# Kernel optimization log

Measured on AMD Instinct MI355X. Metric: run time of the kernel, lower is better.

Reference implementation:

```python
import jax, jax.numpy as jnp
import numpy as np

D_MODEL = 2048
D_STATE = 128
D_CONV = 4
EXPAND = 2
HEADDIM = 64
CHUNK = 64
D_INNER = EXPAND * D_MODEL            # 4096
NHEADS = D_INNER // HEADDIM           # 64
CONV_DIM = D_INNER + 2 * D_STATE      # 4352
D_IN_PROJ = 2 * D_INNER + 2 * D_STATE + NHEADS  # 8512
BATCH, SEQLEN = 2, 2048


def segsum(x):
    """Stable segment sum. x: (..., T) -> (..., T, T)."""
    T = x.shape[-1]
    xx = jnp.broadcast_to(x[..., :, None], x.shape + (T,))  # [.., d, e] = x[.., d]
    mask_lower = jnp.tril(jnp.ones((T, T), dtype=bool), -1)
    s = jnp.cumsum(jnp.where(mask_lower, xx, 0.0), axis=-2)
    mask_diag = jnp.tril(jnp.ones((T, T), dtype=bool), 0)
    return jnp.where(mask_diag, s, -jnp.inf)


def ssd(x, A, Bm, Cm, chunk):
    """x: [b,L,h,p], A: [b,L,h], Bm/Cm: [b,L,n]."""
    b, L, h, p = x.shape
    c = L // chunk
    x = x.reshape(b, c, chunk, h, p)
    A = A.reshape(b, c, chunk, h).transpose(0, 3, 1, 2)     # b h c l
    Bm = Bm.reshape(b, c, chunk, -1)                         # b c l n
    Cm = Cm.reshape(b, c, chunk, -1)
    A_cum = jnp.cumsum(A, axis=-1)                           # b h c l
    Lmat = jnp.exp(segsum(A))                                # b h c l s
    # intra-chunk (diagonal) output
    Y_diag = jnp.einsum('bcln,bcsn,bhcls,bcshp->bclhp', Cm, Bm, Lmat, x)
    # per-chunk states
    decay_states = jnp.exp(A_cum[..., -1:] - A_cum)          # b h c l
    states = jnp.einsum('bcln,bhcl,bclhp->bchpn', Bm, decay_states, x)
    init = jnp.zeros_like(states[:, :1])
    states = jnp.concatenate([init, states], axis=1)         # b (c+1) h p n
    # inter-chunk recurrence via segsum over chunk-level decays
    A_last = jnp.pad(A_cum[..., -1], ((0, 0), (0, 0), (1, 0)))  # b h (c+1)
    decay_chunk = jnp.exp(segsum(A_last))                    # b h (c+1) (c+1)
    new_states = jnp.einsum('bhzc,bchpn->bzhpn', decay_chunk, states)
    states, final_state = new_states[:, :-1], new_states[:, -1]
    # state -> output
    out_decay = jnp.exp(A_cum)                               # b h c l
    Y_off = jnp.einsum('bcln,bchpn,bhcl->bclhp', Cm, states, out_decay)
    return (Y_diag + Y_off).reshape(b, L, h, p), final_state


def setup_inputs() -> dict:
    key = jax.random.key(0)
    ks = jax.random.split(key, 8)
    u = jax.random.normal(ks[0], (BATCH, SEQLEN, D_MODEL), jnp.float32)
    W_in = jax.random.normal(ks[1], (D_MODEL, D_IN_PROJ), jnp.float32) / np.sqrt(D_MODEL).astype(np.float32)
    conv_w = jax.random.normal(ks[2], (CONV_DIM, D_CONV), jnp.float32) * np.sqrt(2.0 / D_CONV).astype(np.float32)
    conv_b = jnp.zeros((CONV_DIM,), jnp.float32)
    dt_bias = jax.random.uniform(ks[3], (NHEADS,), jnp.float32, minval=-2.0, maxval=2.0)
    A_log = jax.random.normal(ks[4], (NHEADS,), jnp.float32) * 0.1
    D_param = jnp.ones((NHEADS,), jnp.float32)
    norm_w = jnp.ones((D_INNER,), jnp.float32)
    W_out = jax.random.normal(ks[5], (D_INNER, D_MODEL), jnp.float32) / np.sqrt(D_INNER).astype(np.float32)
    return {'u': u, 'W_in': W_in, 'conv_w': conv_w, 'conv_b': conv_b,
            'dt_bias': dt_bias, 'A_log': A_log, 'D_param': D_param,
            'norm_w': norm_w, 'W_out': W_out}


def reference(u, W_in, conv_w, conv_b, dt_bias, A_log, D_param, norm_w, W_out):
    b, L, _ = u.shape
    zxbcdt = u @ W_in                                        # [b, L, 2*din + 2*n + h]
    z = zxbcdt[..., :D_INNER]
    xBC = zxbcdt[..., D_INNER:D_INNER + CONV_DIM]
    dt = zxbcdt[..., D_INNER + CONV_DIM:]
    dt = jax.nn.softplus(dt + dt_bias)                       # [b, L, h]
    # causal depthwise conv1d (kernel D_CONV, groups=channels)
    xp = jnp.pad(xBC, ((0, 0), (D_CONV - 1, 0), (0, 0)))
    xBC = sum(xp[:, w:w + L, :] * conv_w[:, w] for w in range(D_CONV)) + conv_b
    xBC = jax.nn.silu(xBC)
    x = xBC[..., :D_INNER]
    Bm = xBC[..., D_INNER:D_INNER + D_STATE]                 # [b, L, n]
    Cm = xBC[..., D_INNER + D_STATE:]                        # [b, L, n]
    x = x.reshape(b, L, NHEADS, HEADDIM)
    A = -jnp.exp(A_log)                                      # [h]
    y, final_state = ssd(x * dt[..., None], A * dt, Bm, Cm, CHUNK)
    y = y + x * D_param[:, None]                             # skip term
    y = y.reshape(b, L, D_INNER)
    # gated RMSNorm (fp32)
    yf = y * jax.nn.silu(z)
    rrms = jax.lax.rsqrt(jnp.mean(yf * yf, axis=-1, keepdims=True) + 1e-5)
    y = yf * rrms * norm_w
    return y @ W_out
```

## Files before the change

kernel.cpp:

```cpp
#include <hip/hip_runtime.h>

typedef unsigned short u16;
typedef __attribute__((ext_vector_type(8))) short bhalf8;
typedef __attribute__((ext_vector_type(4))) float floatx4;

__device__ __forceinline__ u16 f2bf(float f) {
    union { float f; unsigned u; } v; v.f = f;
    unsigned u = v.u;
    unsigned r = u + 0x7fffu + ((u >> 16) & 1u);
    return (u16)(r >> 16);
}
__device__ __forceinline__ float b2f(u16 h) {
    union { unsigned u; float f; } v; v.u = ((unsigned)h) << 16; return v.f;
}
__device__ __forceinline__ void unpack2(unsigned u, float& lo, float& hi) {
    union { unsigned u; float f; } a, b;
    a.u = u << 16; b.u = u & 0xffff0000u;
    lo = a.f; hi = b.f;
}
__device__ __forceinline__ void load_lds16(const void* g, void* l) {
    __builtin_amdgcn_global_load_lds(
        (const __attribute__((address_space(1))) unsigned int*)g,
        (__attribute__((address_space(3))) unsigned int*)l, 16, 0, 0);
}

__global__ void k_f2b4(const float* __restrict__ in, u16* __restrict__ out, int n4) {
    int i = blockIdx.x * 256 + threadIdx.x;
    if (i < n4) {
        float4 v = ((const float4*)in)[i];
        unsigned lo = (unsigned)f2bf(v.x) | ((unsigned)f2bf(v.y) << 16);
        unsigned hi = (unsigned)f2bf(v.z) | ((unsigned)f2bf(v.w) << 16);
        ((uint2*)out)[i] = make_uint2(lo, hi);
    }
}

__global__ void k_transpose_f2b(const float* __restrict__ W, u16* __restrict__ Wt,
                                int K, int N) {
    __shared__ float tile[32][33];
    int nt = blockIdx.x * 32, kt = blockIdx.y * 32;
    int tx = threadIdx.x, ty = threadIdx.y;
    #pragma unroll
    for (int r = 0; r < 32; r += 8) {
        int k = kt + ty + r, n = nt + tx;
        tile[ty + r][tx] = (n < N && k < K) ? W[(size_t)k * N + n] : 0.f;
    }
    __syncthreads();
    #pragma unroll
    for (int r = 0; r < 32; r += 8) {
        int n = nt + ty + r, k = kt + tx;
        Wt[(size_t)n * K + k] = f2bf(tile[tx][ty + r]);
    }
}

template <int EPI>
__global__ __launch_bounds__(256) void gemm_bt(
    const u16* __restrict__ A, const u16* __restrict__ Bt, int M, int N, int K,
    float* __restrict__ outF,
    u16* __restrict__ zb, u16* __restrict__ xbc, float* __restrict__ dtq,
    const float* __restrict__ dt_bias) {
    __shared__ u16 As[128 * 64];
    __shared__ u16 Bs[128 * 64];
    int t = threadIdx.x;
    int w = t >> 6, lane = t & 63;
    int m0 = blockIdx.y * 128, n0 = blockIdx.x * 128;
    int wm = (w >> 1) * 64, wn = (w & 1) * 64;
    floatx4 acc[4][4];
    #pragma unroll
    for (int i = 0; i < 4; i++)
        #pragma unroll
        for (int j = 0; j < 4; j++) acc[i][j] = (floatx4){0.f, 0.f, 0.f, 0.f};

    for (int k0 = 0; k0 < K; k0 += 64) {
        #pragma unroll
        for (int i = 0; i < 4; i++) {
            int c = w * 4 + i;
            int byte = c * 1024 + lane * 16;
            int row = byte >> 7;
            int colb = (byte & 127) ^ ((row & 7) << 4);
            load_lds16(A + (size_t)(m0 + row) * K + k0 + (colb >> 1), (char*)As + byte);
            load_lds16(Bt + (size_t)(n0 + row) * K + k0 + (colb >> 1), (char*)Bs + byte);
        }
        __syncthreads();
        #pragma unroll
        for (int ks = 0; ks < 2; ks++) {
            int kk = ks * 32 + ((lane >> 4) << 3);
            bhalf8 af[4], bf[4];
            #pragma unroll
            for (int mi = 0; mi < 4; mi++) {
                int row = wm + mi * 16 + (lane & 15);
                int idx = (row * 64 + kk) ^ ((row & 7) << 3);
                af[mi] = *(const bhalf8*)(As + idx);
            }
            #pragma unroll
            for (int ni = 0; ni < 4; ni++) {
                int col = wn + ni * 16 + (lane & 15);
                int idx = (col * 64 + kk) ^ ((col & 7) << 3);
                bf[ni] = *(const bhalf8*)(Bs + idx);
            }
            #pragma unroll
            for (int mi = 0; mi < 4; mi++)
                #pragma unroll
                for (int ni = 0; ni < 4; ni++)
                    acc[mi][ni] = __builtin_amdgcn_mfma_f32_16x16x32_bf16(
                        af[mi], bf[ni], acc[mi][ni], 0, 0, 0);
        }
        __syncthreads();
    }
    #pragma unroll
    for (int mi = 0; mi < 4; mi++) {
        #pragma unroll
        for (int ni = 0; ni < 4; ni++) {
            floatx4 v = acc[mi][ni];
            int col = n0 + wn + ni * 16 + (lane & 15);
            #pragma unroll
            for (int r = 0; r < 4; r++) {
                int row = m0 + wm + mi * 16 + ((lane >> 4) << 2) + r;
                float val = v[r];
                if (EPI == 0) {
                    outF[(size_t)row * N + col] = val;
                } else {
                    if (col < 4096) {
                        zb[(size_t)row * 4096 + col] = f2bf(val);
                    } else if (col < 8448) {
                        xbc[(size_t)row * 4352 + (col - 4096)] = f2bf(val);
                    } else if (col < 8512) {
                        int h = col - 8448;
                        float xv = val + dt_bias[h];
                        float sp = (xv > 20.f) ? xv : log1pf(__expf(xv));
                        dtq[(size_t)row * 64 + h] = sp;
                    }
                }
            }
        }
    }
}

__global__ __launch_bounds__(256) void k_conv(
    const u16* __restrict__ xbc, const float* __restrict__ conv_w,
    const float* __restrict__ conv_b,
    u16* __restrict__ x, u16* __restrict__ Bo, u16* __restrict__ Co) {
    int row = blockIdx.x;
    int b = row >> 11, l = row & 2047;
    for (int ch = threadIdx.x; ch < 4352; ch += 256) {
        float acc = conv_b[ch];
        #pragma unroll
        for (int w = 0; w < 4; w++) {
            int ll = l - 3 + w;
            if (ll >= 0) acc += b2f(xbc[(size_t)(b * 2048 + ll) * 4352 + ch]) * conv_w[ch * 4 + w];
        }
        float v = acc / (1.f + __expf(-acc));
        if (ch < 4096) {
            x[(size_t)row * 4096 + ch] = f2bf(v);
        } else if (ch < 4224) {
            Bo[(size_t)row * 128 + (ch - 4096)] = f2bf(v);
        } else {
            Co[(size_t)row * 128 + (ch - 4224)] = f2bf(v);
        }
    }
}

__global__ void k_dtprep(const float* __restrict__ dtq, const float* __restrict__ A_log,
                         float* __restrict__ acum, float* __restrict__ Tc) {
    int bc = blockIdx.x;
    int h = threadIdx.x;
    float A = -__expf(A_log[h]);
    float s = 0.f;
    #pragma unroll
    for (int l = 0; l < 64; l++) {
        int row = bc * 64 + l;
        s += A * dtq[row * 64 + h];
        acum[(size_t)row * 64 + h] = s;
    }
    int b = bc >> 5, c = bc & 31;
    Tc[(b * 64 + h) * 32 + c] = s;
}

__global__ __launch_bounds__(256) void k_G(const u16* __restrict__ Bo, const u16* __restrict__ Co,
                                           float* __restrict__ G) {
    int bc = blockIdx.x;
    __shared__ float BsT[128][68];
    __shared__ float Cs[64][132];
    int t = threadIdx.x;
    for (int idx = t; idx < 64 * 128; idx += 256) {
        int r = idx >> 7, n = idx & 127;
        BsT[n][r] = b2f(Bo[(size_t)(bc * 64 + r) * 128 + n]);
        Cs[r][n] = b2f(Co[(size_t)(bc * 64 + r) * 128 + n]);
    }
    __syncthreads();
    int l = t >> 2, sq = t & 3;
    float a[16];
    #pragma unroll
    for (int i = 0; i < 16; i++) a[i] = 0.f;
    for (int n = 0; n < 128; n++) {
        float cv = Cs[l][n];
        const float4* bp = (const float4*)&BsT[n][sq * 16];
        float4 b0 = bp[0], b1 = bp[1], b2 = bp[2], b3 = bp[3];
        a[0] += cv * b0.x; a[1] += cv * b0.y; a[2] += cv * b0.z; a[3] += cv * b0.w;
        a[4] += cv * b1.x; a[5] += cv * b1.y; a[6] += cv * b1.z; a[7] += cv * b1.w;
        a[8] += cv * b2.x; a[9] += cv * b2.y; a[10] += cv * b2.z; a[11] += cv * b2.w;
        a[12] += cv * b3.x; a[13] += cv * b3.y; a[14] += cv * b3.z; a[15] += cv * b3.w;
    }
    size_t gb = ((size_t)bc * 64 + l) * 64 + sq * 16;
    #pragma unroll
    for (int i = 0; i < 16; i++) G[gb + i] = a[i];
}

__global__ __launch_bounds__(256) void k_diag(
    const u16* __restrict__ xb, const u16* __restrict__ Bo,
    const float* __restrict__ G, const float* __restrict__ acum,
    const float* __restrict__ dtq,
    u16* __restrict__ y, u16* __restrict__ cs) {
    int bc = blockIdx.x, h = blockIdx.y;
    __shared__ u16 XT[4096];
    __shared__ u16 Pl[4096];
    __shared__ u16 BTd[8192];
    __shared__ float ac[64], dec[64], dts[64];
    int t = threadIdx.x, w = t >> 6, lane = t & 63;
    if (t < 64) {
        ac[t] = acum[(size_t)(bc * 64 + t) * 64 + h];
        dts[t] = dtq[(size_t)(bc * 64 + t) * 64 + h];
    }
    __syncthreads();
    if (t < 64) dec[t] = __expf(ac[63] - ac[t]);
    for (int idx = t; idx < 4096; idx += 256) {
        int s = idx >> 6, p = idx & 63;
        float v = b2f(xb[(size_t)(bc * 64 + s) * 4096 + h * 64 + p]) * dts[s];
        XT[(p << 6) + (s ^ ((p & 7) << 3))] = f2bf(v);
    }
    for (int idx = t; idx < 4096; idx += 256) {
        int l = idx >> 6, s = idx & 63;
        float v = (s <= l) ? __expf(ac[l] - ac[s]) * G[((size_t)bc * 64 + l) * 64 + s] : 0.f;
        Pl[(l << 6) + (s ^ ((l & 7) << 3))] = f2bf(v);
    }
    __syncthreads();
    for (int idx = t; idx < 8192; idx += 256) {
        int l = idx >> 7, n = idx & 127;
        float v = b2f(Bo[(size_t)(bc * 64 + l) * 128 + n]) * dec[l];
        BTd[(n << 6) + (l ^ ((n & 7) << 3))] = f2bf(v);
    }
    __syncthreads();
    {
        floatx4 accY[4];
        #pragma unroll
        for (int ni = 0; ni < 4; ni++) accY[ni] = (floatx4){0.f, 0.f, 0.f, 0.f};
        int row = (w << 4) + (lane & 15);
        #pragma unroll
        for (int ks = 0; ks < 2; ks++) {
            int k = (ks << 5) + ((lane >> 4) << 3);
            int kx = k ^ ((row & 7) << 3);
            bhalf8 af = *(const bhalf8*)(Pl + (row << 6) + kx);
            #pragma unroll
            for (int ni = 0; ni < 4; ni++) {
                int pr = (ni << 4) + (lane & 15);
                bhalf8 bf = *(const bhalf8*)(XT + (pr << 6) + kx);
                accY[ni] = __builtin_amdgcn_mfma_f32_16x16x32_bf16(af, bf, accY[ni], 0, 0, 0);
            }
        }
        #pragma unroll
        for (int ni = 0; ni < 4; ni++) {
            int col = (ni << 4) + (lane & 15);
            #pragma unroll
            for (int r = 0; r < 4; r++) {
                int l = (w << 4) + ((lane >> 4) << 2) + r;
                y[(size_t)(bc * 64 + l) * 4096 + h * 64 + col] = f2bf(accY[ni][r]);
            }
        }
    }
    {
        floatx4 accS[8];
        #pragma unroll
        for (int ni = 0; ni < 8; ni++) accS[ni] = (floatx4){0.f, 0.f, 0.f, 0.f};
        int prow = (w << 4) + (lane & 15);
        #pragma unroll
        for (int ks = 0; ks < 2; ks++) {
            int k = (ks << 5) + ((lane >> 4) << 3);
            int kx = k ^ ((prow & 7) << 3);
            bhalf8 af = *(const bhalf8*)(XT + (prow << 6) + kx);
            #pragma unroll
            for (int ni = 0; ni < 8; ni++) {
                int nr = (ni << 4) + (lane & 15);
                bhalf8 bf = *(const bhalf8*)(BTd + (nr << 6) + kx);
                accS[ni] = __builtin_amdgcn_mfma_f32_16x16x32_bf16(af, bf, accS[ni], 0, 0, 0);
            }
        }
        #pragma unroll
        for (int ni = 0; ni < 8; ni++) {
            int n = (ni << 4) + (lane & 15);
            #pragma unroll
            for (int r = 0; r < 4; r++) {
                int p = (w << 4) + ((lane >> 4) << 2) + r;
                cs[((size_t)(bc * 64 + h) * 64 + p) * 128 + n] = f2bf(accS[ni][r]);
            }
        }
    }
}

__global__ __launch_bounds__(256) void k_scan(u16* __restrict__ cs, const float* __restrict__ Tc) {
    int bid = blockIdx.x;
    int bh = bid >> 5, pb = bid & 31;
    int b = bh >> 6, h = bh & 63;
    int pn = pb * 256 + threadIdx.x;
    const float* Tp = Tc + bh * 32;
    size_t stride = (size_t)64 * 8192;
    size_t base = (((size_t)(b * 32) * 64) + h) * 8192 + pn;
    float v[32];
    #pragma unroll
    for (int c = 0; c < 32; c++) v[c] = b2f(cs[base + (size_t)c * stride]);
    float P = 0.f;
    #pragma unroll
    for (int c = 0; c < 32; c++) {
        float tmp = v[c];
        cs[base + (size_t)c * stride] = f2bf(P);
        P = __expf(Tp[c]) * P + tmp;
    }
}

__global__ __launch_bounds__(256) void k_yoff(
    const u16* __restrict__ Co, const u16* __restrict__ cs,
    const float* __restrict__ acum, u16* __restrict__ y) {
    int bc = blockIdx.x, h = blockIdx.y;
    __shared__ u16 Cl[8192];
    __shared__ u16 Sl[8192];
    __shared__ float od[64];
    int t = threadIdx.x, w = t >> 6, lane = t & 63;
    for (int idx = t; idx < 8192; idx += 256) {
        int l = idx >> 7, n = idx & 127;
        Cl[(l << 7) + (n ^ ((l & 15) << 3))] = Co[(size_t)(bc * 64 + l) * 128 + n];
    }
    size_t pbase = ((size_t)bc * 64 + h) * 8192;
    for (int idx = t; idx < 8192; idx += 256) {
        int p = idx >> 7, n = idx & 127;
        Sl[(p << 7) + (n ^ ((p & 15) << 3))] = cs[pbase + idx];
    }
    if (t < 64) od[t] = __expf(acum[(size_t)(bc * 64 + t) * 64 + h]);
    __syncthreads();
    floatx4 acc[4];
    #pragma unroll
    for (int ni = 0; ni < 4; ni++) acc[ni] = (floatx4){0.f, 0.f, 0.f, 0.f};
    int lrow = (w << 4) + (lane & 15);
    #pragma unroll
    for (int ks = 0; ks < 4; ks++) {
        int k = (ks << 5) + ((lane >> 4) << 3);
        int kx = k ^ ((lrow & 15) << 3);
        bhalf8 af = *(const bhalf8*)(Cl + (lrow << 7) + kx);
        #pragma unroll
        for (int ni = 0; ni < 4; ni++) {
            int pr = (ni << 4) + (lane & 15);
            bhalf8 bf = *(const bhalf8*)(Sl + (pr << 7) + kx);
            acc[ni] = __builtin_amdgcn_mfma_f32_16x16x32_bf16(af, bf, acc[ni], 0, 0, 0);
        }
    }
    #pragma unroll
    for (int ni = 0; ni < 4; ni++) {
        int col = (ni << 4) + (lane & 15);
        #pragma unroll
        for (int r = 0; r < 4; r++) {
            int l = (w << 4) + ((lane >> 4) << 2) + r;
            size_t yi = (size_t)(bc * 64 + l) * 4096 + h * 64 + col;
            y[yi] = f2bf(b2f(y[yi]) + od[l] * acc[ni][r]);
        }
    }
}

__global__ __launch_bounds__(256) void k_norm(
    const u16* __restrict__ y, const u16* __restrict__ x, const u16* __restrict__ z,
    const float* __restrict__ D_param, const float* __restrict__ norm_w,
    u16* __restrict__ ynorm) {
    int row = blockIdx.x;
    int t = threadIdx.x;
    size_t base = (size_t)row * 4096 + (size_t)t * 16;
    float yv[16], xf[16], zf[16];
    {
        uint4 a = ((const uint4*)(y + base))[0];
        uint4 b = ((const uint4*)(y + base))[1];
        unpack2(a.x, yv[0], yv[1]); unpack2(a.y, yv[2], yv[3]);
        unpack2(a.z, yv[4], yv[5]); unpack2(a.w, yv[6], yv[7]);
        unpack2(b.x, yv[8], yv[9]); unpack2(b.y, yv[10], yv[11]);
        unpack2(b.z, yv[12], yv[13]); unpack2(b.w, yv[14], yv[15]);
    }
    {
        uint4 a = ((const uint4*)(x + base))[0];
        uint4 b = ((const uint4*)(x + base))[1];
        unpack2(a.x, xf[0], xf[1]); unpack2(a.y, xf[2], xf[3]);
        unpack2(a.z, xf[4], xf[5]); unpack2(a.w, xf[6], xf[7]);
        unpack2(b.x, xf[8], xf[9]); unpack2(b.y, xf[10], xf[11]);
        unpack2(b.z, xf[12], xf[13]); unpack2(b.w, xf[14], xf[15]);
    }
    {
        uint4 a = ((const uint4*)(z + base))[0];
        uint4 b = ((const uint4*)(z + base))[1];
        unpack2(a.x, zf[0], zf[1]); unpack2(a.y, zf[2], zf[3]);
        unpack2(a.z, zf[4], zf[5]); unpack2(a.w, zf[6], zf[7]);
        unpack2(b.x, zf[8], zf[9]); unpack2(b.y, zf[10], zf[11]);
        unpack2(b.z, zf[12], zf[13]); unpack2(b.w, zf[14], zf[15]);
    }
    float D = D_param[t >> 2];
    float vals[16], ss = 0.f;
    #pragma unroll
    for (int j = 0; j < 16; j++) {
        float v = yv[j] + xf[j] * D;
        float zz = zf[j];
        float yf = v * (zz / (1.f + __expf(-zz)));
        vals[j] = yf;
        ss += yf * yf;
    }
    #pragma unroll
    for (int o = 32; o > 0; o >>= 1) ss += __shfl_down(ss, o, 64);
    __shared__ float red[4];
    if ((t & 63) == 0) red[t >> 6] = ss;
    __syncthreads();
    float tot = red[0] + red[1] + red[2] + red[3];
    float rr = rsqrtf(tot * (1.f / 4096.f) + 1e-5f);
    unsigned o32[8];
    #pragma unroll
    for (int j = 0; j < 8; j++) {
        float lo = vals[2 * j] * rr * norm_w[t * 16 + 2 * j];
        float hi = vals[2 * j + 1] * rr * norm_w[t * 16 + 2 * j + 1];
        o32[j] = (unsigned)f2bf(lo) | ((unsigned)f2bf(hi) << 16);
    }
    uint4 w0, w1;
    w0.x = o32[0]; w0.y = o32[1]; w0.z = o32[2]; w0.w = o32[3];
    w1.x = o32[4]; w1.y = o32[5]; w1.z = o32[6]; w1.w = o32[7];
    ((uint4*)(ynorm + base))[0] = w0;
    ((uint4*)(ynorm + base))[1] = w1;
}

extern "C" void kernel_launch(void* const* d_in, const int* in_sizes, int n_in,
                              void* d_out, int out_size, void* d_ws, size_t ws_size,
                              hipStream_t stream) {
    const float* u       = (const float*)d_in[0];
    const float* W_in    = (const float*)d_in[1];
    const float* conv_w  = (const float*)d_in[2];
    const float* conv_b  = (const float*)d_in[3];
    const float* dt_bias = (const float*)d_in[4];
    const float* A_log   = (const float*)d_in[5];
    const float* D_param = (const float*)d_in[6];
    const float* norm_w  = (const float*)d_in[7];
    const float* W_out   = (const float*)d_in[8];
    float* out = (float*)d_out;

    const size_t REGION = (size_t)134217728;
    size_t need = REGION
                + (size_t)33554432
                + (size_t)33554432
                + (size_t)1048576
                + (size_t)1048576
                + (size_t)1048576
                + (size_t)16384
                + (size_t)1048576
                + (size_t)1048576
                + (size_t)33554432;
    if (ws_size < need) return;

    char* ws = (char*)d_ws;
    u16*   ubf   = (u16*)(ws);
    u16*   WinT  = (u16*)(ws + 16777216);
    u16*   xbc   = (u16*)(ws + 16777216 + 35651584);
    u16*   cs    = (u16*)(ws);
    u16*   WoutT = (u16*)(ws);
    u16*   ynorm = (u16*)(ws + 16777216);
    char* p = ws + REGION;
    u16*   zb    = (u16*)p;            p += 33554432;
    u16*   xb    = (u16*)p;            p += 33554432;
    u16*   Bo    = (u16*)p;            p += 1048576;
    u16*   Co    = (u16*)p;            p += 1048576;
    float* acum  = (float*)p;          p += 1048576;
    float* Tc    = (float*)p;          p += 16384;
    float* G     = (float*)p;          p += 1048576;
    float* dtq   = (float*)p;          p += 1048576;
    u16*   yb    = (u16*)p;            p += 33554432;

    k_f2b4<<<8192, 256, 0, stream>>>(u, ubf, 4096 * 2048 / 4);
    k_transpose_f2b<<<dim3(268, 64), dim3(32, 8), 0, stream>>>(W_in, WinT, 2048, 8512);
    gemm_bt<1><<<dim3(67, 32), 256, 0, stream>>>(ubf, WinT, 4096, 8576, 2048,
                                                 nullptr, zb, xbc, dtq, dt_bias);
    k_conv<<<4096, 256, 0, stream>>>(xbc, conv_w, conv_b, xb, Bo, Co);
    k_dtprep<<<64, 64, 0, stream>>>(dtq, A_log, acum, Tc);
    k_G<<<64, 256, 0, stream>>>(Bo, Co, G);
    k_diag<<<dim3(64, 64), 256, 0, stream>>>(xb, Bo, G, acum, dtq, yb, cs);
    k_scan<<<4096, 256, 0, stream>>>(cs, Tc);
    k_yoff<<<dim3(64, 64), 256, 0, stream>>>(Co, cs, acum, yb);
    k_transpose_f2b<<<dim3(64, 128), dim3(32, 8), 0, stream>>>(W_out, WoutT, 4096, 2048);
    k_norm<<<4096, 256, 0, stream>>>(yb, xb, zb, D_param, norm_w, ynorm);
    gemm_bt<0><<<dim3(16, 32), 256, 0, stream>>>(ynorm, WoutT, 4096, 2048, 4096,
                                                 out, nullptr, nullptr, nullptr, nullptr);
    (void)in_sizes; (void)n_in; (void)out_size;
}
```

Baseline: 638.8 us.

## Swizzle GEMM block order, reuse conv history across rows, split k_G over rows

```diff
diff --git a/kernel.cpp b/kernel.cpp
--- a/kernel.cpp
+++ b/kernel.cpp
@@ -55,6 +55,7 @@
 template <int EPI>
 __global__ __launch_bounds__(256) void gemm_bt(
     const u16* __restrict__ A, const u16* __restrict__ Bt, int M, int N, int K,
+    int NT, int GM, int NBW,
     float* __restrict__ outF,
     u16* __restrict__ zb, u16* __restrict__ xbc, float* __restrict__ dtq,
     const float* __restrict__ dt_bias) {
@@ -62,7 +63,16 @@
     __shared__ u16 Bs[128 * 64];
     int t = threadIdx.x;
     int w = t >> 6, lane = t & 63;
-    int m0 = blockIdx.y * 128, n0 = blockIdx.x * 128;
+    int nwg = gridDim.x, bid = blockIdx.x;
+    int swz = (bid & 7) * (nwg >> 3) + (bid >> 3);
+    int sup = GM * NT;
+    int g = swz / sup, r0 = swz % sup;
+    int nb = r0 / (GM * NBW);
+    int rem = r0 - nb * (GM * NBW);
+    int gw = NT - nb * NBW; if (gw > NBW) gw = NBW;
+    int nf = rem % gw, mi = rem / gw;
+    int n_t = nb * NBW + nf, m_t = g * GM + mi;
+    int m0 = m_t * 128, n0 = n_t * 128;
     int wm = (w >> 1) * 64, wn = (w & 1) * 64;
     floatx4 acc[4][4];
     #pragma unroll
@@ -86,10 +96,10 @@
             int kk = ks * 32 + ((lane >> 4) << 3);
             bhalf8 af[4], bf[4];
             #pragma unroll
-            for (int mi = 0; mi < 4; mi++) {
-                int row = wm + mi * 16 + (lane & 15);
+            for (int mi2 = 0; mi2 < 4; mi2++) {
+                int row = wm + mi2 * 16 + (lane & 15);
                 int idx = (row * 64 + kk) ^ ((row & 7) << 3);
-                af[mi] = *(const bhalf8*)(As + idx);
+                af[mi2] = *(const bhalf8*)(As + idx);
             }
             #pragma unroll
             for (int ni = 0; ni < 4; ni++) {
@@ -98,23 +108,23 @@
                 bf[ni] = *(const bhalf8*)(Bs + idx);
             }
             #pragma unroll
-            for (int mi = 0; mi < 4; mi++)
+            for (int mi2 = 0; mi2 < 4; mi2++)
                 #pragma unroll
                 for (int ni = 0; ni < 4; ni++)
-                    acc[mi][ni] = __builtin_amdgcn_mfma_f32_16x16x32_bf16(
-                        af[mi], bf[ni], acc[mi][ni], 0, 0, 0);
+                    acc[mi2][ni] = __builtin_amdgcn_mfma_f32_16x16x32_bf16(
+                        af[mi2], bf[ni], acc[mi2][ni], 0, 0, 0);
         }
         __syncthreads();
     }
     #pragma unroll
-    for (int mi = 0; mi < 4; mi++) {
+    for (int mi2 = 0; mi2 < 4; mi2++) {
         #pragma unroll
         for (int ni = 0; ni < 4; ni++) {
-            floatx4 v = acc[mi][ni];
+            floatx4 v = acc[mi2][ni];
             int col = n0 + wn + ni * 16 + (lane & 15);
             #pragma unroll
             for (int r = 0; r < 4; r++) {
-                int row = m0 + wm + mi * 16 + ((lane >> 4) << 2) + r;
+                int row = m0 + wm + mi2 * 16 + ((lane >> 4) << 2) + r;
                 float val = v[r];
                 if (EPI == 0) {
                     outF[(size_t)row * N + col] = val;
@@ -139,22 +149,32 @@
     const u16* __restrict__ xbc, const float* __restrict__ conv_w,
     const float* __restrict__ conv_b,
     u16* __restrict__ x, u16* __restrict__ Bo, u16* __restrict__ Co) {
-    int row = blockIdx.x;
-    int b = row >> 11, l = row & 2047;
+    int bid = blockIdx.x;
+    int b = bid >> 8, lt = bid & 255;
+    int l0 = lt * 8;
+    size_t rb = (size_t)(b * 2048) * 4352;
     for (int ch = threadIdx.x; ch < 4352; ch += 256) {
-        float acc = conv_b[ch];
-        #pragma unroll
-        for (int w = 0; w < 4; w++) {
-            int ll = l - 3 + w;
-            if (ll >= 0) acc += b2f(xbc[(size_t)(b * 2048 + ll) * 4352 + ch]) * conv_w[ch * 4 + w];
-        }
-        float v = acc / (1.f + __expf(-acc));
-        if (ch < 4096) {
-            x[(size_t)row * 4096 + ch] = f2bf(v);
-        } else if (ch < 4224) {
-            Bo[(size_t)row * 128 + (ch - 4096)] = f2bf(v);
-        } else {
-            Co[(size_t)row * 128 + (ch - 4224)] = f2bf(v);
+        float w0 = conv_w[ch * 4 + 0], w1 = conv_w[ch * 4 + 1];
+        float w2 = conv_w[ch * 4 + 2], w3 = conv_w[ch * 4 + 3];
+        float bc = conv_b[ch];
+        float h0 = (l0 >= 3) ? b2f(xbc[rb + (size_t)(l0 - 3) * 4352 + ch]) : 0.f;
+        float h1 = (l0 >= 2) ? b2f(xbc[rb + (size_t)(l0 - 2) * 4352 + ch]) : 0.f;
+        float h2 = (l0 >= 1) ? b2f(xbc[rb + (size_t)(l0 - 1) * 4352 + ch]) : 0.f;
+        #pragma unroll
+        for (int i = 0; i < 8; i++) {
+            int l = l0 + i;
+            float xc = b2f(xbc[rb + (size_t)l * 4352 + ch]);
+            float acc = bc + w0 * h0 + w1 * h1 + w2 * h2 + w3 * xc;
+            float v = acc / (1.f + __expf(-acc));
+            int row = b * 2048 + l;
+            if (ch < 4096) {
+                x[(size_t)row * 4096 + ch] = f2bf(v);
+            } else if (ch < 4224) {
+                Bo[(size_t)row * 128 + (ch - 4096)] = f2bf(v);
+            } else {
+                Co[(size_t)row * 128 + (ch - 4224)] = f2bf(v);
+            }
+            h0 = h1; h1 = h2; h2 = xc;
         }
     }
 }
@@ -178,31 +198,31 @@
 __global__ __launch_bounds__(256) void k_G(const u16* __restrict__ Bo, const u16* __restrict__ Co,
                                            float* __restrict__ G) {
     int bc = blockIdx.x;
+    int lq = blockIdx.y;
     __shared__ float BsT[128][68];
-    __shared__ float Cs[64][132];
+    __shared__ float Cs[16][132];
     int t = threadIdx.x;
     for (int idx = t; idx < 64 * 128; idx += 256) {
         int r = idx >> 7, n = idx & 127;
         BsT[n][r] = b2f(Bo[(size_t)(bc * 64 + r) * 128 + n]);
-        Cs[r][n] = b2f(Co[(size_t)(bc * 64 + r) * 128 + n]);
-    }
-    __syncthreads();
-    int l = t >> 2, sq = t & 3;
-    float a[16];
-    #pragma unroll
-    for (int i = 0; i < 16; i++) a[i] = 0.f;
+    }
+    for (int idx = t; idx < 16 * 128; idx += 256) {
+        int r = idx >> 7, n = idx & 127;
+        Cs[r][n] = b2f(Co[(size_t)(bc * 64 + lq * 16 + r) * 128 + n]);
+    }
+    __syncthreads();
+    int lr = t >> 4, sq = t & 15;
+    int l = lq * 16 + lr;
+    float a[4] = {0.f, 0.f, 0.f, 0.f};
     for (int n = 0; n < 128; n++) {
-        float cv = Cs[l][n];
-        const float4* bp = (const float4*)&BsT[n][sq * 16];
-        float4 b0 = bp[0], b1 = bp[1], b2 = bp[2], b3 = bp[3];
+        float cv = Cs[lr][n];
+        const float4* bp = (const float4*)&BsT[n][sq * 4];
+        float4 b0 = bp[0];
         a[0] += cv * b0.x; a[1] += cv * b0.y; a[2] += cv * b0.z; a[3] += cv * b0.w;
-        a[4] += cv * b1.x; a[5] += cv * b1.y; a[6] += cv * b1.z; a[7] += cv * b1.w;
-        a[8] += cv * b2.x; a[9] += cv * b2.y; a[10] += cv * b2.z; a[11] += cv * b2.w;
-        a[12] += cv * b3.x; a[13] += cv * b3.y; a[14] += cv * b3.z; a[15] += cv * b3.w;
-    }
-    size_t gb = ((size_t)bc * 64 + l) * 64 + sq * 16;
-    #pragma unroll
-    for (int i = 0; i < 16; i++) G[gb + i] = a[i];
+    }
+    size_t gb = ((size_t)bc * 64 + l) * 64 + sq * 4;
+    #pragma unroll
+    for (int i = 0; i < 4; i++) G[gb + i] = a[i];
 }
 
 __global__ __launch_bounds__(256) void k_diag(
@@ -472,17 +492,17 @@
 
     k_f2b4<<<8192, 256, 0, stream>>>(u, ubf, 4096 * 2048 / 4);
     k_transpose_f2b<<<dim3(268, 64), dim3(32, 8), 0, stream>>>(W_in, WinT, 2048, 8512);
-    gemm_bt<1><<<dim3(67, 32), 256, 0, stream>>>(ubf, WinT, 4096, 8576, 2048,
-                                                 nullptr, zb, xbc, dtq, dt_bias);
-    k_conv<<<4096, 256, 0, stream>>>(xbc, conv_w, conv_b, xb, Bo, Co);
+    gemm_bt<1><<<2144, 256, 0, stream>>>(ubf, WinT, 4096, 8576, 2048, 67, 4, 8,
+                                         nullptr, zb, xbc, dtq, dt_bias);
+    k_conv<<<512, 256, 0, stream>>>(xbc, conv_w, conv_b, xb, Bo, Co);
     k_dtprep<<<64, 64, 0, stream>>>(dtq, A_log, acum, Tc);
-    k_G<<<64, 256, 0, stream>>>(Bo, Co, G);
+    k_G<<<dim3(64, 4), 256, 0, stream>>>(Bo, Co, G);
     k_diag<<<dim3(64, 64), 256, 0, stream>>>(xb, Bo, G, acum, dtq, yb, cs);
     k_scan<<<4096, 256, 0, stream>>>(cs, Tc);
     k_yoff<<<dim3(64, 64), 256, 0, stream>>>(Co, cs, acum, yb);
     k_transpose_f2b<<<dim3(64, 128), dim3(32, 8), 0, stream>>>(W_out, WoutT, 4096, 2048);
     k_norm<<<4096, 256, 0, stream>>>(yb, xb, zb, D_param, norm_w, ynorm);
-    gemm_bt<0><<<dim3(16, 32), 256, 0, stream>>>(ynorm, WoutT, 4096, 2048, 4096,
-                                                 out, nullptr, nullptr, nullptr, nullptr);
+    gemm_bt<0><<<512, 256, 0, stream>>>(ynorm, WoutT, 4096, 2048, 4096, 16, 4, 4,
+                                        out, nullptr, nullptr, nullptr, nullptr);
     (void)in_sizes; (void)n_in; (void)out_size;
 }
```

New measurement: 663.4 us. 1.04x slower.
